# Kernel tuning notes

Hardware: AMD Instinct MI355X
Metric: run time of the kernel (lower is better)

Reference implementation:

```python
import jax, jax.numpy as jnp
import numpy as np

NUM_CLASSES = 64  # K: fill_max for class ids c


def setup_inputs() -> dict:
    key = jax.random.key(0)
    k1, k2 = jax.random.split(key)
    z = jax.random.normal(k1, (16, 8192, 256), dtype=jnp.float32)
    c = jax.random.randint(k2, (16, 8192), 0, NUM_CLASSES, dtype=jnp.int64)
    return {"z": z, "c": c}


def reference(z, c):
    # z: [B, S, D], c: [B, S] int class ids in [0, K)
    D = z.shape[-1]
    zf = z.reshape(-1, D)          # [N, D]
    cf = c.reshape(-1)             # [N]
    N = zf.shape[0]

    # Fused segmented reductions instead of a python loop over unique ids.
    counts = jax.ops.segment_sum(jnp.ones((N,), zf.dtype), cf, num_segments=NUM_CLASSES)  # [K]
    sums = jax.ops.segment_sum(zf, cf, num_segments=NUM_CLASSES)                          # [K, D]
    safe_counts = jnp.maximum(counts, 1.0)
    centroids = sums / safe_counts[:, None]                                               # [K, D] per-class mean

    # within-class variance: mean squared distance of members to their centroid
    diff = zf - centroids[cf]                                                             # [N, D] gather
    sq = jnp.sum(diff * diff, axis=-1)                                                    # [N]
    var_withins = jax.ops.segment_sum(sq, cf, num_segments=NUM_CLASSES) / safe_counts     # [K]

    return centroids, var_withins
```

## Files before the change

### kernel.cpp

```cpp
#include <hip/hip_runtime.h>
#include <hip/hip_bf16.h>

#define K_CLS 64
#define DIM   256
#define TPB1  512
#define MAXROWS 2048

typedef __attribute__((ext_vector_type(8)))  short short8;
typedef __attribute__((ext_vector_type(16))) float f32x16;
typedef __attribute__((ext_vector_type(4)))  unsigned int uint4v;

__device__ inline float bf2f(unsigned short h) {
    return __uint_as_float(((unsigned)h) << 16);
}
__device__ inline unsigned short f2bf(float x) {
    unsigned u = __float_as_uint(x);
    u += 0x7FFFu + ((u >> 16) & 1u);
    return (unsigned short)(u >> 16);
}
__device__ inline unsigned int pkbf(float lo, float hi) {
    float2 p; p.x = lo; p.y = hi;
    __hip_bfloat162 h = __float22bfloat162_rn(p);
    unsigned int r;
    __builtin_memcpy(&r, &h, sizeof(r));
    return r;
}

__global__ __launch_bounds__(TPB1) void fstat_p1(
    const float* __restrict__ z, const int* __restrict__ c,
    unsigned short* __restrict__ psum, unsigned short* __restrict__ psq,
    float* __restrict__ pcnt, float* __restrict__ out,
    int rows_per_blk, int nblk)
{
    __shared__ __align__(16) int cs[MAXROWS];
    __shared__ float lcnt[K_CLS];
    const int t   = threadIdx.x;
    const int blk = blockIdx.x;
    const int rb0 = blk * rows_per_blk;

    if (blk == 0 && t < K_CLS) out[K_CLS * DIM + t] = 0.f;

    if (t < K_CLS) lcnt[t] = 0.f;
    __syncthreads();
    for (int r = t; r < rows_per_blk; r += TPB1) {
        int cv = c[rb0 + r];
        cs[r] = cv;
        atomicAdd(&lcnt[cv], 1.0f);
    }
    __syncthreads();

    const int wave = t >> 6;
    const int lane = t & 63;
    const int db   = wave * 32;
    const int half = lane >> 5;
    const int ln   = lane & 31;
    const int ln32 = ln + 32;

    f32x16 aS0 = {}; f32x16 aS1 = {}; f32x16 aQ0 = {}; f32x16 aQ1 = {};

    const int nsteps = rows_per_blk >> 4;
    const size_t zo0 = (size_t)(rb0 + half * 8) * DIM + db + ln;

    float v[8];
    #pragma unroll
    for (int i = 0; i < 8; ++i) v[i] = z[zo0 + (size_t)i * DIM];

    for (int step = 0; step < nsteps; ++step) {
        float vn[8];
        if (step + 1 < nsteps) {
            const size_t zo = zo0 + (size_t)(step + 1) * 16 * DIM;
            #pragma unroll
            for (int i = 0; i < 8; ++i) vn[i] = z[zo + (size_t)i * DIM];
        }
        const int rb = step * 16 + half * 8;
        int4 c0 = *reinterpret_cast<const int4*>(&cs[rb]);
        int4 c1 = *reinterpret_cast<const int4*>(&cs[rb + 4]);
        int cl[8] = {c0.x, c0.y, c0.z, c0.w, c1.x, c1.y, c1.z, c1.w};

        uint4v ua0, ua1, ubz, ubq;
        #pragma unroll
        for (int i = 0; i < 4; ++i) {
            int l0 = cl[2 * i], l1 = cl[2 * i + 1];
            ua0[i] = (l0 == ln   ? 0x00003F80u : 0u) | (l1 == ln   ? 0x3F800000u : 0u);
            ua1[i] = (l0 == ln32 ? 0x00003F80u : 0u) | (l1 == ln32 ? 0x3F800000u : 0u);
            float v0 = v[2 * i], v1 = v[2 * i + 1];
            ubz[i] = pkbf(v0, v1);
            ubq[i] = pkbf(v0 * v0, v1 * v1);
        }
        short8 A0 = __builtin_bit_cast(short8, ua0);
        short8 A1 = __builtin_bit_cast(short8, ua1);
        short8 Bz = __builtin_bit_cast(short8, ubz);
        short8 Bq = __builtin_bit_cast(short8, ubq);

        aS0 = __builtin_amdgcn_mfma_f32_32x32x16_bf16(A0, Bz, aS0, 0, 0, 0);
        aS1 = __builtin_amdgcn_mfma_f32_32x32x16_bf16(A1, Bz, aS1, 0, 0, 0);
        aQ0 = __builtin_amdgcn_mfma_f32_32x32x16_bf16(A0, Bq, aQ0, 0, 0, 0);
        aQ1 = __builtin_amdgcn_mfma_f32_32x32x16_bf16(A1, Bq, aQ1, 0, 0, 0);
        if (step + 1 < nsteps) {
            #pragma unroll
            for (int i = 0; i < 8; ++i) v[i] = vn[i];
        }
    }

    unsigned short* ps = psum + (size_t)blk * K_CLS * DIM;
    unsigned short* pq = psq  + (size_t)blk * K_CLS * DIM;
    #pragma unroll
    for (int r = 0; r < 16; ++r) {
        int row = (r & 3) + 8 * (r >> 2) + 4 * half;
        size_t o0 = (size_t)row * DIM + db + ln;
        size_t o1 = (size_t)(row + 32) * DIM + db + ln;
        ps[o0] = f2bf(aS0[r]); ps[o1] = f2bf(aS1[r]);
        pq[o0] = f2bf(aQ0[r]); pq[o1] = f2bf(aQ1[r]);
    }
    __syncthreads();
    if (t < K_CLS) pcnt[(size_t)t * nblk + blk] = lcnt[t];
}

__global__ __launch_bounds__(1024) void fstat_p2(
    const unsigned short* __restrict__ psum, const unsigned short* __restrict__ psq,
    const float* __restrict__ pcnt, float* __restrict__ out, int nblk)
{
    const int k  = blockIdx.x >> 2;
    const int q  = blockIdx.x & 3;
    const int t  = threadIdx.x;
    const int d  = t & 63;
    const int sg = t >> 6;

    __shared__ float redS[16][64];
    __shared__ float redQ[16][64];
    __shared__ float redC[256];
    __shared__ float sh_cnt;

    if (t < 256) redC[t] = (t < nblk) ? pcnt[(size_t)k * nblk + t] : 0.f;
    __syncthreads();
    if (t < 64) {
        float cp = redC[t] + redC[t + 64] + redC[t + 128] + redC[t + 192];
        #pragma unroll
        for (int off = 32; off > 0; off >>= 1) cp += __shfl_down(cp, off);
        if (t == 0) sh_cnt = cp;
    }

    float s = 0.f, qq = 0.f;
    for (int b = sg; b < nblk; b += 16) {
        size_t o = ((size_t)b * K_CLS + k) * DIM + q * 64 + d;
        s  += bf2f(psum[o]);
        qq += bf2f(psq[o]);
    }
    redS[sg][d] = s;
    redQ[sg][d] = qq;
    __syncthreads();

    if (t < 64) {
        float su = 0.f, qu = 0.f;
        #pragma unroll
        for (int i = 0; i < 16; ++i) { su += redS[i][t]; qu += redQ[i][t]; }
        float cnt = fmaxf(sh_cnt, 1.f);
        float mu  = su / cnt;
        out[(size_t)k * DIM + q * 64 + t] = mu;
        float vp = qu / cnt - mu * mu;
        #pragma unroll
        for (int off = 32; off > 0; off >>= 1) vp += __shfl_down(vp, off);
        if (t == 0) atomicAdd(&out[K_CLS * DIM + k], vp);
    }
}

extern "C" void kernel_launch(void* const* d_in, const int* in_sizes, int n_in,
                              void* d_out, int out_size, void* d_ws, size_t ws_size,
                              hipStream_t stream)
{
    const float* z = (const float*)d_in[0];
    const int*   c = (const int*)d_in[1];
    float* out = (float*)d_out;
    const int N = in_sizes[1];

    auto need = [](int nb) {
        return 2 * (size_t)nb * K_CLS * DIM * sizeof(unsigned short)
             + (size_t)K_CLS * nb * sizeof(float);
    };
    int nblk = 256;
    while (nblk > 64 &&
           (N % nblk != 0 || (N / nblk) % 16 != 0 || (N / nblk) > MAXROWS ||
            need(nblk) > ws_size))
        nblk >>= 1;

    const int rows_per_blk = N / nblk;

    unsigned short* psum = (unsigned short*)d_ws;
    unsigned short* psq  = psum + (size_t)nblk * K_CLS * DIM;
    float* pcnt = (float*)(psq + (size_t)nblk * K_CLS * DIM);

    fstat_p1<<<nblk, TPB1, 0, stream>>>(z, c, psum, psq, pcnt, out, rows_per_blk, nblk);
    fstat_p2<<<K_CLS * 4, 1024, 0, stream>>>(psum, psq, pcnt, out, nblk);
}
```

Baseline: 36.28 us.

## Stage z tiles through LDS with async global_load_lds double buffering

Replaces the per-thread register prefetch of z rows with asynchronous global-to-LDS DMA (global_load_lds, 16 bytes per lane) into two 16-row LDS buffers, double-buffered across steps. Each step issues the next tile's load, reads the current tile from LDS, runs the MFMAs, then waits at a block barrier. The aim is to cut vector register pressure and let the memory system stream z more directly. In exchange it adds 32 KB of LDS and a full block barrier every step. It also relies on the barrier draining the async loads before the buffer is reused, and prefetch depth stays at one tile.

```diff
diff --git a/kernel.cpp b/kernel.cpp
--- a/kernel.cpp
+++ b/kernel.cpp
@@ -9,6 +9,14 @@
 typedef __attribute__((ext_vector_type(8)))  short short8;
 typedef __attribute__((ext_vector_type(16))) float f32x16;
 typedef __attribute__((ext_vector_type(4)))  unsigned int uint4v;
+
+#define AS1 __attribute__((address_space(1)))
+#define AS3 __attribute__((address_space(3)))
+
+__device__ inline void gld16(const void* g, void* l) {
+    __builtin_amdgcn_global_load_lds((const AS1 unsigned int*)g,
+                                     (AS3 unsigned int*)l, 16, 0, 0);
+}
 
 __device__ inline float bf2f(unsigned short h) {
     return __uint_as_float(((unsigned)h) << 16);
@@ -34,6 +42,8 @@
 {
     __shared__ __align__(16) int cs[MAXROWS];
     __shared__ float lcnt[K_CLS];
+    __shared__ __align__(16) float zt0[16 * DIM];
+    __shared__ __align__(16) float zt1[16 * DIM];
     const int t   = threadIdx.x;
     const int blk = blockIdx.x;
     const int rb0 = blk * rows_per_blk;
@@ -47,7 +57,6 @@
         cs[r] = cv;
         atomicAdd(&lcnt[cv], 1.0f);
     }
-    __syncthreads();
 
     const int wave = t >> 6;
     const int lane = t & 63;
@@ -55,27 +64,36 @@
     const int half = lane >> 5;
     const int ln   = lane & 31;
     const int ln32 = ln + 32;
+    const int soff = wave * 1024 + lane * 16;
+
+    const float* zblk = z + (size_t)rb0 * DIM;
+    auto stage = [&](float* dst, int step) {
+        const char* g = (const char*)(zblk + (size_t)step * 16 * DIM);
+        char* l = (char*)dst;
+        gld16(g + soff, l + soff);
+        gld16(g + 8192 + soff, l + 8192 + soff);
+    };
 
     f32x16 aS0 = {}; f32x16 aS1 = {}; f32x16 aQ0 = {}; f32x16 aQ1 = {};
 
     const int nsteps = rows_per_blk >> 4;
-    const size_t zo0 = (size_t)(rb0 + half * 8) * DIM + db + ln;
-
-    float v[8];
-    #pragma unroll
-    for (int i = 0; i < 8; ++i) v[i] = z[zo0 + (size_t)i * DIM];
+
+    stage(zt0, 0);
+    __syncthreads();
 
     for (int step = 0; step < nsteps; ++step) {
-        float vn[8];
-        if (step + 1 < nsteps) {
-            const size_t zo = zo0 + (size_t)(step + 1) * 16 * DIM;
-            #pragma unroll
-            for (int i = 0; i < 8; ++i) vn[i] = z[zo + (size_t)i * DIM];
-        }
+        float* curb = (step & 1) ? zt1 : zt0;
+        float* nxtb = (step & 1) ? zt0 : zt1;
+        if (step + 1 < nsteps) stage(nxtb, step + 1);
+
         const int rb = step * 16 + half * 8;
         int4 c0 = *reinterpret_cast<const int4*>(&cs[rb]);
         int4 c1 = *reinterpret_cast<const int4*>(&cs[rb + 4]);
         int cl[8] = {c0.x, c0.y, c0.z, c0.w, c1.x, c1.y, c1.z, c1.w};
+
+        float v[8];
+        #pragma unroll
+        for (int i = 0; i < 8; ++i) v[i] = curb[(half * 8 + i) * DIM + db + ln];
 
         uint4v ua0, ua1, ubz, ubq;
         #pragma unroll
@@ -96,10 +114,8 @@
         aS1 = __builtin_amdgcn_mfma_f32_32x32x16_bf16(A1, Bz, aS1, 0, 0, 0);
         aQ0 = __builtin_amdgcn_mfma_f32_32x32x16_bf16(A0, Bq, aQ0, 0, 0, 0);
         aQ1 = __builtin_amdgcn_mfma_f32_32x32x16_bf16(A1, Bq, aQ1, 0, 0, 0);
-        if (step + 1 < nsteps) {
-            #pragma unroll
-            for (int i = 0; i < 8; ++i) v[i] = vn[i];
-        }
+
+        __syncthreads();
     }
 
     unsigned short* ps = psum + (size_t)blk * K_CLS * DIM;
@@ -112,7 +128,6 @@
         ps[o0] = f2bf(aS0[r]); ps[o1] = f2bf(aS1[r]);
         pq[o0] = f2bf(aQ0[r]); pq[o1] = f2bf(aQ1[r]);
     }
-    __syncthreads();
     if (t < K_CLS) pcnt[(size_t)t * nblk + blk] = lcnt[t];
 }
 
```

New measurement: 41.23 us. 1.14x slower.
